# Performance work log

Measured on AMD Instinct MI355X. Metric: run time of the kernel, lower is better.

## Reference

```python
import jax, jax.numpy as jnp
import numpy as np

G = 56      # voxel grid side
N = 60000   # active voxels
K = 27      # 3x3x3 kernel offsets
CIN, COUT = 64, 96


def _build_kernel_map(seed=0):
    """Host-side hash-map neighbor search (what spnn does internally).
    Returns in_idx/out_idx of shape (K, N); padded entries have out_idx == N
    (scattered into a trash row) and in_idx == 0 (any valid gather index)."""
    rng = np.random.default_rng(seed)
    flat = rng.choice(G ** 3, size=N, replace=False)
    coords = np.stack(np.unravel_index(flat, (G, G, G)), axis=1)  # (N, 3)
    lut = -np.ones(G ** 3, dtype=np.int64)
    lut[flat] = np.arange(N)
    offs = np.array([(dx, dy, dz) for dx in (-1, 0, 1)
                     for dy in (-1, 0, 1) for dz in (-1, 0, 1)])
    in_idx = np.zeros((K, N), dtype=np.int32)
    out_idx = np.full((K, N), N, dtype=np.int32)
    for k in range(K):
        nb = coords + offs[k]
        ok = np.all((nb >= 0) & (nb < G), axis=1)
        fl = np.clip(nb[:, 0] * G * G + nb[:, 1] * G + nb[:, 2], 0, G ** 3 - 1)
        j = np.where(ok, lut[fl], -1)
        sel = np.nonzero(j >= 0)[0]
        m = sel.shape[0]
        out_idx[k, :m] = sel.astype(np.int32)       # output point i
        in_idx[k, :m] = j[sel].astype(np.int32)     # its neighbor at offset k
    return jnp.asarray(in_idx), jnp.asarray(out_idx)


def setup_inputs() -> dict:
    key = jax.random.key(0)
    ks = jax.random.split(key, 10)
    in_idx, out_idx = _build_kernel_map(0)
    s1 = 1.0 / np.sqrt(K * CIN)
    s2 = 1.0 / np.sqrt(K * COUT)
    return {
        "x":  jax.random.normal(ks[0], (N, CIN), jnp.float32),
        "W1": jax.random.normal(ks[1], (K, CIN, COUT), jnp.float32) * s1,
        "g1": jnp.ones((COUT,), jnp.float32),
        "b1": jnp.zeros((COUT,), jnp.float32),
        "m1": jax.random.normal(ks[2], (COUT,), jnp.float32) * 0.1,
        "v1": jax.random.uniform(ks[3], (COUT,), jnp.float32, 0.5, 1.5),
        "W2": jax.random.normal(ks[4], (K, COUT, COUT), jnp.float32) * s2,
        "g2": jnp.ones((COUT,), jnp.float32),
        "b2": jnp.zeros((COUT,), jnp.float32),
        "m2": jax.random.normal(ks[5], (COUT,), jnp.float32) * 0.1,
        "v2": jax.random.uniform(ks[6], (COUT,), jnp.float32, 0.5, 1.5),
        "Wd": jax.random.normal(ks[7], (CIN, COUT), jnp.float32) / np.sqrt(CIN),
        "gd": jnp.ones((COUT,), jnp.float32),
        "bd": jnp.zeros((COUT,), jnp.float32),
        "md": jax.random.normal(ks[8], (COUT,), jnp.float32) * 0.1,
        "vd": jax.random.uniform(ks[9], (COUT,), jnp.float32, 0.5, 1.5),
        "in_idx": in_idx,
        "out_idx": out_idx,
    }


def _bn(h, g, b, m, v, eps=1e-5):
    return (h - m) * (g * jax.lax.rsqrt(v + eps)) + b


def _sparse_conv(feat, W, in_idx, out_idx):
    # gather -> GEMM -> scatter-add, one pass per kernel offset.
    n = feat.shape[0]
    out = jnp.zeros((n + 1, W.shape[2]), feat.dtype)  # row n = trash row
    for k in range(W.shape[0]):
        out = out.at[out_idx[k]].add(feat[in_idx[k]] @ W[k])
    return out[:n]


def reference(x, W1, g1, b1, m1, v1, W2, g2, b2, m2, v2,
              Wd, gd, bd, md, vd, in_idx, out_idx):
    h = jax.nn.relu(_bn(_sparse_conv(x, W1, in_idx, out_idx), g1, b1, m1, v1))
    h = _bn(_sparse_conv(h, W2, in_idx, out_idx), g2, b2, m2, v2)
    skip = _bn(x @ Wd, gd, bd, md, vd)  # 1x1 conv downsample (inc != outc)
    return jax.nn.relu(h + skip)
```

## Files before the change

### kernel.cpp

```cpp
#include <hip/hip_runtime.h>


typedef __attribute__((ext_vector_type(8))) short bf16x8;
typedef __attribute__((ext_vector_type(4))) float f32x4;
typedef unsigned short u16;

constexpr int K27  = 27;
constexpr int CIN  = 64;
constexpr int COUT = 96;
constexpr int W1SZ = 6144;
constexpr int W2SZ = 9216;

#define MFMA __builtin_amdgcn_mfma_f32_16x16x32_bf16

__device__ __forceinline__ u16 f2bf(float f) {
  unsigned u = __float_as_uint(f);
  return (u16)((u + 0x7FFFu + ((u >> 16) & 1u)) >> 16);
}

__device__ __forceinline__ int posf(int c) {
  return ((c >> 2) & 3) * 8 + (c & 3) + ((c >> 4) & 1) * 4;
}

__device__ __forceinline__ bf16x8 ld16(const u16* p) {
  union { bf16x8 f; uint4 u; } r;
  r.u = *reinterpret_cast<const uint4*>(p);
  return r.f;
}

__device__ __forceinline__ void gll(const u16* g, u16* l) {
  __builtin_amdgcn_global_load_lds(
      (const __attribute__((address_space(1))) unsigned int*)g,
      (__attribute__((address_space(3))) unsigned int*)l, 16, 0, 0);
}

__device__ __forceinline__ void stage1(const u16* g, u16* l, int t) {
#pragma unroll
  for (int s = 0; s < 3; ++s) gll(g + s * 2048 + t * 8, l + s * 2048 + t * 8);
}

__device__ __forceinline__ void stage2(const u16* g, u16* l, int t) {
#pragma unroll
  for (int s = 0; s < 4; ++s) gll(g + s * 2048 + t * 8, l + s * 2048 + t * 8);
  if (t < 128) gll(g + 8192 + t * 8, l + 8192 + t * 8);
}

__device__ __forceinline__ int xcd_swz(int bid, int nblk) {
  int q = nblk >> 3, r = nblk & 7;
  int x = bid & 7, i = bid >> 3;
  return (x < r ? x * (q + 1) : r * (q + 1) + (x - r) * q) + i;
}

__global__ void build_nbT(const int* __restrict__ in_idx, const int* __restrict__ out_idx,
                          int* __restrict__ nbT, int N, int N_pad) {
  int t = blockIdx.x * blockDim.x + threadIdx.x;
  if (t >= K27 * N) return;
  int k = t / N;
  int o = out_idx[t];
  if (o < N) nbT[(size_t)k * N_pad + o] = in_idx[t];
}

__global__ void prep_all(
    const float* __restrict__ x, const float* __restrict__ W1,
    const float* __restrict__ W2, const float* __restrict__ Wd,
    const float* g1, const float* b1, const float* m1, const float* v1,
    const float* g2, const float* b2, const float* m2, const float* v2,
    const float* gd, const float* bd, const float* md, const float* vd,
    u16* __restrict__ xbf, u16* __restrict__ W1t, u16* __restrict__ W2t,
    u16* __restrict__ Wdt, float* __restrict__ bnc, u16* __restrict__ hbf, int N) {
  long i = (long)blockIdx.x * blockDim.x + threadIdx.x;
  const long R0 = (long)(N + 1) * CIN;
  const long R1 = (long)K27 * W1SZ;
  const long R2 = (long)K27 * W2SZ;
  const long R3 = (long)CIN * COUT;
  if (i < R0) {
    int c = (int)(i & 63);
    float v = (i < (long)N * CIN) ? x[i] : 0.f;
    xbf[(i & ~63L) + (c & 32) + posf(c & 31)] = f2bf(v);
    return;
  }
  i -= R0;
  if (i < R1) {
    int k = (int)(i / W1SZ), r = (int)(i % W1SZ);
    int f = r >> 9, lane = (r >> 3) & 63, j = r & 7;
    int c = f / 6, n = f % 6, m = lane & 15, g = lane >> 4;
    int co = n * 16 + m;
    int ci = c * 32 + 4 * g + (j & 3) + 16 * (j >> 2);
    W1t[i] = f2bf(W1[((size_t)k * CIN + ci) * COUT + co]);
    return;
  }
  i -= R1;
  if (i < R2) {
    int k = (int)(i / W2SZ), r = (int)(i % W2SZ);
    int f = r >> 9, lane = (r >> 3) & 63, j = r & 7;
    int c = f / 6, n = f % 6, m = lane & 15, g = lane >> 4;
    int co = n * 16 + m;
    int ci = c * 32 + 4 * g + (j & 3) + 16 * (j >> 2);
    W2t[i] = f2bf(W2[((size_t)k * COUT + ci) * COUT + co]);
    return;
  }
  i -= R2;
  if (i < R3) {
    int ci = (int)(i / COUT), co = (int)(i % COUT);
    Wdt[co * CIN + (ci & 32) + posf(ci & 31)] = f2bf(Wd[i]);
    return;
  }
  i -= R3;
  if (i < COUT) {
    int c = (int)i;
    float A1 = g1[c] * rsqrtf(v1[c] + 1e-5f);
    float A2 = g2[c] * rsqrtf(v2[c] + 1e-5f);
    float Ad = gd[c] * rsqrtf(vd[c] + 1e-5f);
    bnc[c]       = A1;
    bnc[96 + c]  = b1[c] - m1[c] * A1;
    bnc[192 + c] = A2;
    bnc[288 + c] = b2[c] - m2[c] * A2 + bd[c] - md[c] * Ad;
    bnc[384 + c] = Ad / A2;
    hbf[(size_t)N * COUT + c] = 0;
  }
}

__global__ __launch_bounds__(256, 2) void conv1_mfma(
    const u16* __restrict__ xbf, const u16* __restrict__ W1t,
    const int* __restrict__ nbT, const float* __restrict__ bnc,
    u16* __restrict__ hbf, int N, int N_pad) {
  __shared__ u16 Blds[2][W1SZ];
  const int t    = threadIdx.x;
  const int lane = t & 63;
  const int m    = lane & 15;
  const int slot = lane >> 4;
  const int so   = slot * 8;
  const int wid  = t >> 6;
  const int wr   = wid >> 1;
  const int wc   = wid & 1;
  const int bswz = xcd_swz(blockIdx.x, gridDim.x);
  const int roww = bswz * 64 + wr * 32;

  f32x4 acc[2][3];
#pragma unroll
  for (int s = 0; s < 2; ++s)
#pragma unroll
    for (int n = 0; n < 3; ++n) acc[s][n] = (f32x4){0.f, 0.f, 0.f, 0.f};

  const int* nbp = nbT + roww + m;

  stage1(W1t, Blds[0], t);
  int j1a = nbp[N_pad],               j1b = nbp[N_pad + 16];
  int j2a = nbp[2 * (size_t)N_pad],   j2b = nbp[2 * (size_t)N_pad + 16];
  bf16x8 Aa[2][2], Ab[2][2];
  {
    int j0a = nbp[0], j0b = nbp[16];
    const u16* pa = xbf + (size_t)(j0a < 0 ? N : j0a) * CIN + so;
    const u16* pb = xbf + (size_t)(j0b < 0 ? N : j0b) * CIN + so;
    Aa[0][0] = ld16(pa); Aa[0][1] = ld16(pa + 32);
    Aa[1][0] = ld16(pb); Aa[1][1] = ld16(pb + 32);
  }
  __syncthreads();

  auto step = [&](int k, bf16x8 (&Ac)[2][2], bf16x8 (&An)[2][2]) {
    const int cur = k & 1;
    if (k + 1 < K27) stage1(W1t + (size_t)(k + 1) * W1SZ, Blds[cur ^ 1], t);
    int j3a = 0, j3b = 0;
    if (k + 3 < K27) {
      j3a = nbp[(size_t)(k + 3) * N_pad];
      j3b = nbp[(size_t)(k + 3) * N_pad + 16];
    }
    if (k + 1 < K27) {
      const u16* pa = xbf + (size_t)(j1a < 0 ? N : j1a) * CIN + so;
      const u16* pb = xbf + (size_t)(j1b < 0 ? N : j1b) * CIN + so;
      An[0][0] = ld16(pa); An[0][1] = ld16(pa + 32);
      An[1][0] = ld16(pb); An[1][1] = ld16(pb + 32);
    }
    j1a = j2a; j1b = j2b; j2a = j3a; j2b = j3b;
    const u16* Bb = Blds[cur] + wc * 1536 + lane * 8;
#pragma unroll
    for (int c = 0; c < 2; ++c)
#pragma unroll
      for (int nn = 0; nn < 3; ++nn) {
        bf16x8 B = ld16(Bb + (c * 6 + nn) * 512);
        acc[0][nn] = MFMA(Ac[0][c], B, acc[0][nn], 0, 0, 0);
        acc[1][nn] = MFMA(Ac[1][c], B, acc[1][nn], 0, 0, 0);
      }
    __syncthreads();
  };

  for (int kk = 0; kk < K27 - 1; kk += 2) {
    step(kk, Aa, Ab);
    step(kk + 1, Ab, Aa);
  }
  step(K27 - 1, Aa, Ab);

  const int pbase = ((m >> 2) << 3) + (m & 3);
#pragma unroll
  for (int nn = 0; nn < 3; ++nn) {
    const int n   = wc * 3 + nn;
    const int col = n * 16 + m;
    const int dcol = (n >> 1) * 32 + pbase + ((n & 1) << 2);
    const float sc = bnc[col], bi = bnc[COUT + col];
#pragma unroll
    for (int s = 0; s < 2; ++s)
#pragma unroll
      for (int r = 0; r < 4; ++r) {
        const int row = roww + s * 16 + slot * 4 + r;
        if (row < N)
          hbf[(size_t)row * COUT + dcol] = f2bf(fmaxf(fmaf(acc[s][nn][r], sc, bi), 0.f));
      }
  }
}

__global__ __launch_bounds__(256, 2) void conv2_mfma(
    const u16* __restrict__ hbf, const u16* __restrict__ W2t,
    const u16* __restrict__ xbf, const u16* __restrict__ Wdt,
    const int* __restrict__ nbT, const float* __restrict__ bnc,
    float* __restrict__ out, int N, int N_pad) {
  __shared__ u16 Blds[2][W2SZ];
  const int t    = threadIdx.x;
  const int lane = t & 63;
  const int m    = lane & 15;
  const int slot = lane >> 4;
  const int so   = slot * 8;
  const int wid  = t >> 6;
  const int wr   = wid >> 1;
  const int wc   = wid & 1;
  const int bswz = xcd_swz(blockIdx.x, gridDim.x);
  const int roww = bswz * 64 + wr * 32;

  f32x4 acc[2][3];
#pragma unroll
  for (int s = 0; s < 2; ++s)
#pragma unroll
    for (int n = 0; n < 3; ++n) acc[s][n] = (f32x4){0.f, 0.f, 0.f, 0.f};

  stage2(W2t, Blds[0], t);

  {
    int r0 = roww + m, r1 = roww + 16 + m;
    const u16* pa = xbf + (size_t)(r0 < N ? r0 : N) * CIN + so;
    const u16* pb = xbf + (size_t)(r1 < N ? r1 : N) * CIN + so;
    bf16x8 S0a = ld16(pa), S1a = ld16(pa + 32);
    bf16x8 S0b = ld16(pb), S1b = ld16(pb + 32);
#pragma unroll
    for (int nn = 0; nn < 3; ++nn) {
      const int col = (wc * 3 + nn) * 16 + m;
      const u16* wd = Wdt + col * CIN + so;
      bf16x8 B0 = ld16(wd), B1 = ld16(wd + 32);
      acc[0][nn] = MFMA(S0a, B0, acc[0][nn], 0, 0, 0);
      acc[0][nn] = MFMA(S1a, B1, acc[0][nn], 0, 0, 0);
      acc[1][nn] = MFMA(S0b, B0, acc[1][nn], 0, 0, 0);
      acc[1][nn] = MFMA(S1b, B1, acc[1][nn], 0, 0, 0);
    }
#pragma unroll
    for (int nn = 0; nn < 3; ++nn) {
      float rr = bnc[384 + (wc * 3 + nn) * 16 + m];
      acc[0][nn] *= rr;
      acc[1][nn] *= rr;
    }
  }

  const int* nbp = nbT + roww + m;
  int j1a = nbp[N_pad],             j1b = nbp[N_pad + 16];
  int j2a = nbp[2 * (size_t)N_pad], j2b = nbp[2 * (size_t)N_pad + 16];
  bf16x8 Aa[2][3], Ab[2][3];
  {
    int j0a = nbp[0], j0b = nbp[16];
    const u16* pa = hbf + (size_t)(j0a < 0 ? N : j0a) * COUT + so;
    const u16* pb = hbf + (size_t)(j0b < 0 ? N : j0b) * COUT + so;
    Aa[0][0] = ld16(pa); Aa[0][1] = ld16(pa + 32); Aa[0][2] = ld16(pa + 64);
    Aa[1][0] = ld16(pb); Aa[1][1] = ld16(pb + 32); Aa[1][2] = ld16(pb + 64);
  }
  __syncthreads();

  auto step = [&](int k, bf16x8 (&Ac)[2][3], bf16x8 (&An)[2][3]) {
    const int cur = k & 1;
    if (k + 1 < K27) stage2(W2t + (size_t)(k + 1) * W2SZ, Blds[cur ^ 1], t);
    int j3a = 0, j3b = 0;
    if (k + 3 < K27) {
      j3a = nbp[(size_t)(k + 3) * N_pad];
      j3b = nbp[(size_t)(k + 3) * N_pad + 16];
    }
    if (k + 1 < K27) {
      const u16* pa = hbf + (size_t)(j1a < 0 ? N : j1a) * COUT + so;
      const u16* pb = hbf + (size_t)(j1b < 0 ? N : j1b) * COUT + so;
      An[0][0] = ld16(pa); An[0][1] = ld16(pa + 32); An[0][2] = ld16(pa + 64);
      An[1][0] = ld16(pb); An[1][1] = ld16(pb + 32); An[1][2] = ld16(pb + 64);
    }
    j1a = j2a; j1b = j2b; j2a = j3a; j2b = j3b;
    const u16* Bb = Blds[cur] + wc * 1536 + lane * 8;
#pragma unroll
    for (int c = 0; c < 3; ++c)
#pragma unroll
      for (int nn = 0; nn < 3; ++nn) {
        bf16x8 B = ld16(Bb + (c * 6 + nn) * 512);
        acc[0][nn] = MFMA(Ac[0][c], B, acc[0][nn], 0, 0, 0);
        acc[1][nn] = MFMA(Ac[1][c], B, acc[1][nn], 0, 0, 0);
      }
    __syncthreads();
  };

  for (int kk = 0; kk < K27 - 1; kk += 2) {
    step(kk, Aa, Ab);
    step(kk + 1, Ab, Aa);
  }
  step(K27 - 1, Aa, Ab);

#pragma unroll
  for (int nn = 0; nn < 3; ++nn) {
    const int col = (wc * 3 + nn) * 16 + m;
    const float sc = bnc[192 + col], bi = bnc[288 + col];
#pragma unroll
    for (int s = 0; s < 2; ++s)
#pragma unroll
      for (int r = 0; r < 4; ++r) {
        const int row = roww + s * 16 + slot * 4 + r;
        if (row < N)
          out[(size_t)row * COUT + col] = fmaxf(fmaf(acc[s][nn][r], sc, bi), 0.f);
      }
  }
}

extern "C" void kernel_launch(void* const* d_in, const int* in_sizes, int n_in,
                              void* d_out, int out_size, void* d_ws, size_t ws_size,
                              hipStream_t stream) {
  const float* x  = (const float*)d_in[0];
  const float* W1 = (const float*)d_in[1];
  const float* g1 = (const float*)d_in[2];
  const float* b1 = (const float*)d_in[3];
  const float* m1 = (const float*)d_in[4];
  const float* v1 = (const float*)d_in[5];
  const float* W2 = (const float*)d_in[6];
  const float* g2 = (const float*)d_in[7];
  const float* b2 = (const float*)d_in[8];
  const float* m2 = (const float*)d_in[9];
  const float* v2 = (const float*)d_in[10];
  const float* Wd = (const float*)d_in[11];
  const float* gd = (const float*)d_in[12];
  const float* bd = (const float*)d_in[13];
  const float* md = (const float*)d_in[14];
  const float* vd = (const float*)d_in[15];
  const int* in_idx  = (const int*)d_in[16];
  const int* out_idx = (const int*)d_in[17];

  const int N  = in_sizes[0] / CIN;
  const int GB = (N + 63) / 64;
  const int N_pad = GB * 64;

  char* ws = (char*)d_ws;
  size_t off = 0;
  auto alloc = [&](size_t bytes) { size_t o = off; off = (off + bytes + 255) & ~(size_t)255; return o; };
  int*   nbT = (int*)(ws + alloc((size_t)K27 * N_pad * sizeof(int)));
  u16*   xbf = (u16*)(ws + alloc((size_t)(N + 1) * CIN * sizeof(u16)));
  u16*   hbf = (u16*)(ws + alloc((size_t)(N + 1) * COUT * sizeof(u16)));
  u16*   W1t = (u16*)(ws + alloc((size_t)K27 * W1SZ * sizeof(u16)));
  u16*   W2t = (u16*)(ws + alloc((size_t)K27 * W2SZ * sizeof(u16)));
  u16*   Wdt = (u16*)(ws + alloc((size_t)COUT * CIN * sizeof(u16)));
  float* bnc = (float*)(ws + alloc(5 * 96 * sizeof(float)));

  hipMemsetAsync(nbT, 0xFF, (size_t)K27 * N_pad * sizeof(int), stream);
  build_nbT<<<(K27 * N + 255) / 256, 256, 0, stream>>>(in_idx, out_idx, nbT, N, N_pad);

  long ptotal = (long)(N + 1) * CIN + (long)K27 * W1SZ + (long)K27 * W2SZ +
                (long)CIN * COUT + COUT;
  prep_all<<<(int)((ptotal + 255) / 256), 256, 0, stream>>>(
      x, W1, W2, Wd, g1, b1, m1, v1, g2, b2, m2, v2, gd, bd, md, vd,
      xbf, W1t, W2t, Wdt, bnc, hbf, N);

  conv1_mfma<<<GB, 256, 0, stream>>>(xbf, W1t, nbT, bnc, hbf, N, N_pad);
  conv2_mfma<<<GB, 256, 0, stream>>>(hbf, W2t, xbf, Wdt, nbT, bnc, (float*)d_out, N, N_pad);
}
```

Before: 136.5 us.

## Replace full syncthreads with partial vmcnt waits and branchless padded prefetch pipeline

Replaces __syncthreads in the conv main loops with an explicit s_waitcnt vmcnt(N) plus s_barrier, so the next step's gather loads stay in flight across the barrier. Pads the neighbor table to 30 offsets and the weight buffers by one extra slice, which lets the k+1/k+3 guards be dropped and gives a branchless loop. Adds sched_barriers to pin instruction order. The hand-set vmcnt values depend on the exact load count per step (including stage1/stage2 global loads), so a wrong count could race on LDS. The padded weight slice is never initialised but is only staged and never used.

```diff
diff --git a/kernel.cpp b/kernel.cpp
--- a/kernel.cpp
+++ b/kernel.cpp
@@ -6,6 +6,7 @@
 typedef unsigned short u16;
 
 constexpr int K27  = 27;
+constexpr int KPAD = 30;
 constexpr int CIN  = 64;
 constexpr int COUT = 96;
 constexpr int W1SZ = 6144;
@@ -145,32 +146,34 @@
   const int* nbp = nbT + roww + m;
 
   stage1(W1t, Blds[0], t);
-  int j1a = nbp[N_pad],               j1b = nbp[N_pad + 16];
-  int j2a = nbp[2 * (size_t)N_pad],   j2b = nbp[2 * (size_t)N_pad + 16];
+  __builtin_amdgcn_sched_barrier(0);
+  int j1a, j1b, j2a, j2b;
   bf16x8 Aa[2][2], Ab[2][2];
   {
     int j0a = nbp[0], j0b = nbp[16];
+    j1a = nbp[N_pad];               j1b = nbp[N_pad + 16];
+    j2a = nbp[2 * (size_t)N_pad];   j2b = nbp[2 * (size_t)N_pad + 16];
     const u16* pa = xbf + (size_t)(j0a < 0 ? N : j0a) * CIN + so;
     const u16* pb = xbf + (size_t)(j0b < 0 ? N : j0b) * CIN + so;
     Aa[0][0] = ld16(pa); Aa[0][1] = ld16(pa + 32);
     Aa[1][0] = ld16(pb); Aa[1][1] = ld16(pb + 32);
   }
-  __syncthreads();
+  asm volatile("s_waitcnt vmcnt(6)" ::: "memory");
+  __builtin_amdgcn_s_barrier();
+  __builtin_amdgcn_sched_barrier(0);
 
   auto step = [&](int k, bf16x8 (&Ac)[2][2], bf16x8 (&An)[2][2]) {
     const int cur = k & 1;
-    if (k + 1 < K27) stage1(W1t + (size_t)(k + 1) * W1SZ, Blds[cur ^ 1], t);
-    int j3a = 0, j3b = 0;
-    if (k + 3 < K27) {
-      j3a = nbp[(size_t)(k + 3) * N_pad];
-      j3b = nbp[(size_t)(k + 3) * N_pad + 16];
-    }
-    if (k + 1 < K27) {
+    stage1(W1t + (size_t)(k + 1) * W1SZ, Blds[cur ^ 1], t);
+    __builtin_amdgcn_sched_barrier(0);
+    {
       const u16* pa = xbf + (size_t)(j1a < 0 ? N : j1a) * CIN + so;
       const u16* pb = xbf + (size_t)(j1b < 0 ? N : j1b) * CIN + so;
       An[0][0] = ld16(pa); An[0][1] = ld16(pa + 32);
       An[1][0] = ld16(pb); An[1][1] = ld16(pb + 32);
     }
+    int j3a = nbp[(size_t)(k + 3) * N_pad];
+    int j3b = nbp[(size_t)(k + 3) * N_pad + 16];
     j1a = j2a; j1b = j2b; j2a = j3a; j2b = j3b;
     const u16* Bb = Blds[cur] + wc * 1536 + lane * 8;
 #pragma unroll
@@ -181,7 +184,9 @@
         acc[0][nn] = MFMA(Ac[0][c], B, acc[0][nn], 0, 0, 0);
         acc[1][nn] = MFMA(Ac[1][c], B, acc[1][nn], 0, 0, 0);
       }
-    __syncthreads();
+    asm volatile("s_waitcnt vmcnt(6)" ::: "memory");
+    __builtin_amdgcn_s_barrier();
+    __builtin_amdgcn_sched_barrier(0);
   };
 
   for (int kk = 0; kk < K27 - 1; kk += 2) {
@@ -189,6 +194,8 @@
     step(kk + 1, Ab, Aa);
   }
   step(K27 - 1, Aa, Ab);
+  asm volatile("" :: "v"(Ab[0][0]), "v"(Ab[0][1]), "v"(Ab[1][0]), "v"(Ab[1][1]),
+                     "v"(j1a), "v"(j1b), "v"(j2a), "v"(j2b));
 
   const int pbase = ((m >> 2) << 3) + (m & 3);
 #pragma unroll
@@ -232,7 +239,7 @@
     for (int n = 0; n < 3; ++n) acc[s][n] = (f32x4){0.f, 0.f, 0.f, 0.f};
 
   stage2(W2t, Blds[0], t);
-
+  __builtin_amdgcn_sched_barrier(0);
   {
     int r0 = roww + m, r1 = roww + 16 + m;
     const u16* pa = xbf + (size_t)(r0 < N ? r0 : N) * CIN + so;
@@ -258,32 +265,33 @@
   }
 
   const int* nbp = nbT + roww + m;
-  int j1a = nbp[N_pad],             j1b = nbp[N_pad + 16];
-  int j2a = nbp[2 * (size_t)N_pad], j2b = nbp[2 * (size_t)N_pad + 16];
+  int j1a, j1b, j2a, j2b;
   bf16x8 Aa[2][3], Ab[2][3];
   {
     int j0a = nbp[0], j0b = nbp[16];
+    j1a = nbp[N_pad];               j1b = nbp[N_pad + 16];
+    j2a = nbp[2 * (size_t)N_pad];   j2b = nbp[2 * (size_t)N_pad + 16];
     const u16* pa = hbf + (size_t)(j0a < 0 ? N : j0a) * COUT + so;
     const u16* pb = hbf + (size_t)(j0b < 0 ? N : j0b) * COUT + so;
     Aa[0][0] = ld16(pa); Aa[0][1] = ld16(pa + 32); Aa[0][2] = ld16(pa + 64);
     Aa[1][0] = ld16(pb); Aa[1][1] = ld16(pb + 32); Aa[1][2] = ld16(pb + 64);
   }
-  __syncthreads();
+  asm volatile("s_waitcnt vmcnt(8)" ::: "memory");
+  __builtin_amdgcn_s_barrier();
+  __builtin_amdgcn_sched_barrier(0);
 
   auto step = [&](int k, bf16x8 (&Ac)[2][3], bf16x8 (&An)[2][3]) {
     const int cur = k & 1;
-    if (k + 1 < K27) stage2(W2t + (size_t)(k + 1) * W2SZ, Blds[cur ^ 1], t);
-    int j3a = 0, j3b = 0;
-    if (k + 3 < K27) {
-      j3a = nbp[(size_t)(k + 3) * N_pad];
-      j3b = nbp[(size_t)(k + 3) * N_pad + 16];
-    }
-    if (k + 1 < K27) {
+    stage2(W2t + (size_t)(k + 1) * W2SZ, Blds[cur ^ 1], t);
+    __builtin_amdgcn_sched_barrier(0);
+    {
       const u16* pa = hbf + (size_t)(j1a < 0 ? N : j1a) * COUT + so;
       const u16* pb = hbf + (size_t)(j1b < 0 ? N : j1b) * COUT + so;
       An[0][0] = ld16(pa); An[0][1] = ld16(pa + 32); An[0][2] = ld16(pa + 64);
       An[1][0] = ld16(pb); An[1][1] = ld16(pb + 32); An[1][2] = ld16(pb + 64);
     }
+    int j3a = nbp[(size_t)(k + 3) * N_pad];
+    int j3b = nbp[(size_t)(k + 3) * N_pad + 16];
     j1a = j2a; j1b = j2b; j2a = j3a; j2b = j3b;
     const u16* Bb = Blds[cur] + wc * 1536 + lane * 8;
 #pragma unroll
@@ -294,7 +302,9 @@
         acc[0][nn] = MFMA(Ac[0][c], B, acc[0][nn], 0, 0, 0);
         acc[1][nn] = MFMA(Ac[1][c], B, acc[1][nn], 0, 0, 0);
       }
-    __syncthreads();
+    asm volatile("s_waitcnt vmcnt(8)" ::: "memory");
+    __builtin_amdgcn_s_barrier();
+    __builtin_amdgcn_sched_barrier(0);
   };
 
   for (int kk = 0; kk < K27 - 1; kk += 2) {
@@ -302,6 +312,9 @@
     step(kk + 1, Ab, Aa);
   }
   step(K27 - 1, Aa, Ab);
+  asm volatile("" :: "v"(Ab[0][0]), "v"(Ab[0][1]), "v"(Ab[0][2]),
+                     "v"(Ab[1][0]), "v"(Ab[1][1]), "v"(Ab[1][2]),
+                     "v"(j1a), "v"(j1b), "v"(j2a), "v"(j2b));
 
 #pragma unroll
   for (int nn = 0; nn < 3; ++nn) {
@@ -347,15 +360,15 @@
   char* ws = (char*)d_ws;
   size_t off = 0;
   auto alloc = [&](size_t bytes) { size_t o = off; off = (off + bytes + 255) & ~(size_t)255; return o; };
-  int*   nbT = (int*)(ws + alloc((size_t)K27 * N_pad * sizeof(int)));
+  int*   nbT = (int*)(ws + alloc((size_t)KPAD * N_pad * sizeof(int)));
   u16*   xbf = (u16*)(ws + alloc((size_t)(N + 1) * CIN * sizeof(u16)));
   u16*   hbf = (u16*)(ws + alloc((size_t)(N + 1) * COUT * sizeof(u16)));
-  u16*   W1t = (u16*)(ws + alloc((size_t)K27 * W1SZ * sizeof(u16)));
-  u16*   W2t = (u16*)(ws + alloc((size_t)K27 * W2SZ * sizeof(u16)));
+  u16*   W1t = (u16*)(ws + alloc((size_t)(K27 + 1) * W1SZ * sizeof(u16)));
+  u16*   W2t = (u16*)(ws + alloc((size_t)(K27 + 1) * W2SZ * sizeof(u16)));
   u16*   Wdt = (u16*)(ws + alloc((size_t)COUT * CIN * sizeof(u16)));
   float* bnc = (float*)(ws + alloc(5 * 96 * sizeof(float)));
 
-  hipMemsetAsync(nbT, 0xFF, (size_t)K27 * N_pad * sizeof(int), stream);
+  hipMemsetAsync(nbT, 0xFF, (size_t)KPAD * N_pad * sizeof(int), stream);
   build_nbT<<<(K27 * N + 255) / 256, 256, 0, stream>>>(in_idx, out_idx, nbT, N, N_pad);
 
   long ptotal = (long)(N + 1) * CIN + (long)K27 * W1SZ + (long)K27 * W2SZ +
```

Measured after the change: 138.8 us. Within noise of the previous version (+1.8%).

## Stage gathered A rows into swizzled LDS via async global_load_lds

Applied to the files above, without the earlier changes.

Replaces the per-lane register prefetch of gathered neighbor rows with asynchronous global-to-LDS loads into an XOR-swizzled shared tile, then reads the A fragments from LDS for the MFMAs. The neighbor table is padded to 32 offsets so index prefetch two steps ahead needs no bounds check, and the hbf zero row is extended for the padded column chunks. It also raises wave priority around the MFMA block. The aim is to cut register pressure and issue the irregular gathers as wide coalesced async copies, at the cost of an extra barrier per offset step and more LDS use.

```diff
diff --git a/kernel.cpp b/kernel.cpp
--- a/kernel.cpp
+++ b/kernel.cpp
@@ -6,6 +6,7 @@
 typedef unsigned short u16;
 
 constexpr int K27  = 27;
+constexpr int KPAD = 32;
 constexpr int CIN  = 64;
 constexpr int COUT = 96;
 constexpr int W1SZ = 6144;
@@ -32,17 +33,6 @@
   __builtin_amdgcn_global_load_lds(
       (const __attribute__((address_space(1))) unsigned int*)g,
       (__attribute__((address_space(3))) unsigned int*)l, 16, 0, 0);
-}
-
-__device__ __forceinline__ void stage1(const u16* g, u16* l, int t) {
-#pragma unroll
-  for (int s = 0; s < 3; ++s) gll(g + s * 2048 + t * 8, l + s * 2048 + t * 8);
-}
-
-__device__ __forceinline__ void stage2(const u16* g, u16* l, int t) {
-#pragma unroll
-  for (int s = 0; s < 4; ++s) gll(g + s * 2048 + t * 8, l + s * 2048 + t * 8);
-  if (t < 128) gll(g + 8192 + t * 8, l + 8192 + t * 8);
 }
 
 __device__ __forceinline__ int xcd_swz(int bid, int nblk) {
@@ -106,17 +96,19 @@
     return;
   }
   i -= R3;
-  if (i < COUT) {
-    int c = (int)i;
-    float A1 = g1[c] * rsqrtf(v1[c] + 1e-5f);
-    float A2 = g2[c] * rsqrtf(v2[c] + 1e-5f);
-    float Ad = gd[c] * rsqrtf(vd[c] + 1e-5f);
-    bnc[c]       = A1;
-    bnc[96 + c]  = b1[c] - m1[c] * A1;
-    bnc[192 + c] = A2;
-    bnc[288 + c] = b2[c] - m2[c] * A2 + bd[c] - md[c] * Ad;
-    bnc[384 + c] = Ad / A2;
-    hbf[(size_t)N * COUT + c] = 0;
+  if (i < 128) {
+    hbf[(size_t)N * COUT + i] = 0;
+    if (i < COUT) {
+      int c = (int)i;
+      float A1 = g1[c] * rsqrtf(v1[c] + 1e-5f);
+      float A2 = g2[c] * rsqrtf(v2[c] + 1e-5f);
+      float Ad = gd[c] * rsqrtf(vd[c] + 1e-5f);
+      bnc[c]       = A1;
+      bnc[96 + c]  = b1[c] - m1[c] * A1;
+      bnc[192 + c] = A2;
+      bnc[288 + c] = b2[c] - m2[c] * A2 + bd[c] - md[c] * Ad;
+      bnc[384 + c] = Ad / A2;
+    }
   }
 }
 
@@ -124,17 +116,17 @@
     const u16* __restrict__ xbf, const u16* __restrict__ W1t,
     const int* __restrict__ nbT, const float* __restrict__ bnc,
     u16* __restrict__ hbf, int N, int N_pad) {
-  __shared__ u16 Blds[2][W1SZ];
+  __shared__ u16 Ab[4096];
+  __shared__ u16 Bb[2][W1SZ];
   const int t    = threadIdx.x;
   const int lane = t & 63;
   const int m    = lane & 15;
   const int slot = lane >> 4;
-  const int so   = slot * 8;
-  const int wid  = t >> 6;
-  const int wr   = wid >> 1;
-  const int wc   = wid & 1;
-  const int bswz = xcd_swz(blockIdx.x, gridDim.x);
-  const int roww = bswz * 64 + wr * 32;
+  const int w    = t >> 6;
+  const int wr   = w >> 1;
+  const int wc   = w & 1;
+  const int row0 = xcd_swz(blockIdx.x, gridDim.x) * 64;
+  const int roww = row0 + wr * 32;
 
   f32x4 acc[2][3];
 #pragma unroll
@@ -142,53 +134,76 @@
 #pragma unroll
     for (int n = 0; n < 3; ++n) acc[s][n] = (f32x4){0.f, 0.f, 0.f, 0.f};
 
-  const int* nbp = nbT + roww + m;
-
-  stage1(W1t, Blds[0], t);
-  int j1a = nbp[N_pad],               j1b = nbp[N_pad + 16];
-  int j2a = nbp[2 * (size_t)N_pad],   j2b = nbp[2 * (size_t)N_pad + 16];
-  bf16x8 Aa[2][2], Ab[2][2];
-  {
-    int j0a = nbp[0], j0b = nbp[16];
-    const u16* pa = xbf + (size_t)(j0a < 0 ? N : j0a) * CIN + so;
-    const u16* pb = xbf + (size_t)(j0b < 0 ? N : j0b) * CIN + so;
-    Aa[0][0] = ld16(pa); Aa[0][1] = ld16(pa + 32);
-    Aa[1][0] = ld16(pb); Aa[1][1] = ld16(pb + 32);
-  }
+  int rA[2], qsw[2];
+#pragma unroll
+  for (int i = 0; i < 2; ++i) {
+    int c = (w * 2 + i) * 64 + lane;
+    int r = c >> 3;
+    rA[i]  = r;
+    qsw[i] = ((c & 7) ^ (r & 7)) * 8;
+  }
+
+  auto loadJ = [&](int kt, int (&jd)[2]) {
+#pragma unroll
+    for (int i = 0; i < 2; ++i) jd[i] = nbT[(size_t)kt * N_pad + row0 + rA[i]];
+  };
+  auto stageA = [&](int (&jc)[2]) {
+#pragma unroll
+    for (int i = 0; i < 2; ++i) {
+      int j = jc[i];
+      const u16* src = xbf + (size_t)(j < 0 ? N : j) * CIN + qsw[i];
+      gll(src, (u16*)Ab + (w * 2 + i) * 512);
+    }
+  };
+  auto stageB = [&](int kt) {
+#pragma unroll
+    for (int s = 0; s < 3; ++s)
+      gll(W1t + (size_t)kt * W1SZ + s * 2048 + t * 8, &Bb[kt & 1][s * 2048 + t * 8]);
+  };
+  auto compute = [&](int k) {
+    const u16* Bc = Bb[k & 1] + wc * 1536 + lane * 8;
+    bf16x8 av[2][2];
+#pragma unroll
+    for (int s = 0; s < 2; ++s) {
+      const int row = wr * 32 + s * 16 + m;
+      const u16* ar = (const u16*)Ab + row * 64;
+      const int rx = row & 7;
+#pragma unroll
+      for (int c = 0; c < 2; ++c) av[s][c] = ld16(ar + ((slot + c * 4) ^ rx) * 8);
+    }
+    __builtin_amdgcn_s_setprio(1);
+#pragma unroll
+    for (int c = 0; c < 2; ++c)
+#pragma unroll
+      for (int nn = 0; nn < 3; ++nn) {
+        bf16x8 B = ld16(Bc + (c * 6 + nn) * 512);
+        acc[0][nn] = MFMA(av[0][c], B, acc[0][nn], 0, 0, 0);
+        acc[1][nn] = MFMA(av[1][c], B, acc[1][nn], 0, 0, 0);
+      }
+    __builtin_amdgcn_s_setprio(0);
+  };
+
+  int jA[2], jB[2];
+  loadJ(0, jA);
+  stageB(0);
+  stageA(jA);
+  loadJ(1, jA);
   __syncthreads();
 
-  auto step = [&](int k, bf16x8 (&Ac)[2][2], bf16x8 (&An)[2][2]) {
-    const int cur = k & 1;
-    if (k + 1 < K27) stage1(W1t + (size_t)(k + 1) * W1SZ, Blds[cur ^ 1], t);
-    int j3a = 0, j3b = 0;
-    if (k + 3 < K27) {
-      j3a = nbp[(size_t)(k + 3) * N_pad];
-      j3b = nbp[(size_t)(k + 3) * N_pad + 16];
-    }
-    if (k + 1 < K27) {
-      const u16* pa = xbf + (size_t)(j1a < 0 ? N : j1a) * CIN + so;
-      const u16* pb = xbf + (size_t)(j1b < 0 ? N : j1b) * CIN + so;
-      An[0][0] = ld16(pa); An[0][1] = ld16(pa + 32);
-      An[1][0] = ld16(pb); An[1][1] = ld16(pb + 32);
-    }
-    j1a = j2a; j1b = j2b; j2a = j3a; j2b = j3b;
-    const u16* Bb = Blds[cur] + wc * 1536 + lane * 8;
-#pragma unroll
-    for (int c = 0; c < 2; ++c)
-#pragma unroll
-      for (int nn = 0; nn < 3; ++nn) {
-        bf16x8 B = ld16(Bb + (c * 6 + nn) * 512);
-        acc[0][nn] = MFMA(Ac[0][c], B, acc[0][nn], 0, 0, 0);
-        acc[1][nn] = MFMA(Ac[1][c], B, acc[1][nn], 0, 0, 0);
-      }
+  auto step = [&](int k, int (&jc)[2], int (&jn)[2]) {
+    if (k + 1 < K27) stageB(k + 1);
+    loadJ(k + 2, jn);
+    compute(k);
     __syncthreads();
+    if (k + 1 < K27) stageA(jc);
+    __syncthreads();
   };
 
   for (int kk = 0; kk < K27 - 1; kk += 2) {
-    step(kk, Aa, Ab);
-    step(kk + 1, Ab, Aa);
-  }
-  step(K27 - 1, Aa, Ab);
+    step(kk,     jA, jB);
+    step(kk + 1, jB, jA);
+  }
+  step(K27 - 1, jA, jB);
 
   const int pbase = ((m >> 2) << 3) + (m & 3);
 #pragma unroll
@@ -213,17 +228,17 @@
     const u16* __restrict__ xbf, const u16* __restrict__ Wdt,
     const int* __restrict__ nbT, const float* __restrict__ bnc,
     float* __restrict__ out, int N, int N_pad) {
-  __shared__ u16 Blds[2][W2SZ];
+  __shared__ u16 Ab[8192];
+  __shared__ u16 Bb[2][W2SZ];
   const int t    = threadIdx.x;
   const int lane = t & 63;
   const int m    = lane & 15;
   const int slot = lane >> 4;
-  const int so   = slot * 8;
-  const int wid  = t >> 6;
-  const int wr   = wid >> 1;
-  const int wc   = wid & 1;
-  const int bswz = xcd_swz(blockIdx.x, gridDim.x);
-  const int roww = bswz * 64 + wr * 32;
+  const int w    = t >> 6;
+  const int wr   = w >> 1;
+  const int wc   = w & 1;
+  const int row0 = xcd_swz(blockIdx.x, gridDim.x) * 64;
+  const int roww = row0 + wr * 32;
 
   f32x4 acc[2][3];
 #pragma unroll
@@ -231,18 +246,76 @@
 #pragma unroll
     for (int n = 0; n < 3; ++n) acc[s][n] = (f32x4){0.f, 0.f, 0.f, 0.f};
 
-  stage2(W2t, Blds[0], t);
+  int rA[4], qsw[4], inv[4];
+#pragma unroll
+  for (int i = 0; i < 4; ++i) {
+    int c = (w * 4 + i) * 64 + lane;
+    int r = c >> 4;
+    int q = (c & 15) ^ (r & 7);
+    rA[i]  = r;
+    qsw[i] = q * 8;
+    inv[i] = (q >= 12);
+  }
+
+  auto loadJ = [&](int kt, int (&jd)[4]) {
+#pragma unroll
+    for (int i = 0; i < 4; ++i) jd[i] = nbT[(size_t)kt * N_pad + row0 + rA[i]];
+  };
+  auto stageA = [&](int (&jc)[4]) {
+#pragma unroll
+    for (int i = 0; i < 4; ++i) {
+      int j = jc[i];
+      int sel = (j < 0 || inv[i]) ? N : j;
+      const u16* src = hbf + (size_t)sel * COUT + qsw[i];
+      gll(src, (u16*)Ab + (w * 4 + i) * 512);
+    }
+  };
+  auto stageB = [&](int kt) {
+    const u16* src = W2t + (size_t)kt * W2SZ;
+    u16* dst = Bb[kt & 1];
+#pragma unroll
+    for (int s = 0; s < 4; ++s) gll(src + s * 2048 + t * 8, dst + s * 2048 + t * 8);
+    if (t < 128) gll(src + 8192 + t * 8, dst + 8192 + t * 8);
+  };
+  auto compute = [&](int k) {
+    const u16* Bc = Bb[k & 1] + wc * 1536 + lane * 8;
+    bf16x8 av[2][3];
+#pragma unroll
+    for (int s = 0; s < 2; ++s) {
+      const int row = wr * 32 + s * 16 + m;
+      const u16* ar = (const u16*)Ab + row * 128;
+      const int rx = row & 7;
+#pragma unroll
+      for (int c = 0; c < 3; ++c) av[s][c] = ld16(ar + ((slot + c * 4) ^ rx) * 8);
+    }
+    __builtin_amdgcn_s_setprio(1);
+#pragma unroll
+    for (int c = 0; c < 3; ++c)
+#pragma unroll
+      for (int nn = 0; nn < 3; ++nn) {
+        bf16x8 B = ld16(Bc + (c * 6 + nn) * 512);
+        acc[0][nn] = MFMA(av[0][c], B, acc[0][nn], 0, 0, 0);
+        acc[1][nn] = MFMA(av[1][c], B, acc[1][nn], 0, 0, 0);
+      }
+    __builtin_amdgcn_s_setprio(0);
+  };
+
+  int jA[4], jB[4];
+  loadJ(0, jA);
+  stageB(0);
+  stageA(jA);
+  loadJ(1, jA);
 
   {
     int r0 = roww + m, r1 = roww + 16 + m;
-    const u16* pa = xbf + (size_t)(r0 < N ? r0 : N) * CIN + so;
-    const u16* pb = xbf + (size_t)(r1 < N ? r1 : N) * CIN + so;
+    const u16* pa = xbf + (size_t)(r0 < N ? r0 : N) * CIN + slot * 8;
+    const u16* pb = xbf + (size_t)(r1 < N ? r1 : N) * CIN + slot * 8;
     bf16x8 S0a = ld16(pa), S1a = ld16(pa + 32);
     bf16x8 S0b = ld16(pb), S1b = ld16(pb + 32);
 #pragma unroll
     for (int nn = 0; nn < 3; ++nn) {
       const int col = (wc * 3 + nn) * 16 + m;
-      const u16* wd = Wdt + col * CIN + so;
+      const u16* wd = Wdt + col * CIN + slot * 8;
       bf16x8 B0 = ld16(wd), B1 = ld16(wd + 32);
       acc[0][nn] = MFMA(S0a, B0, acc[0][nn], 0, 0, 0);
       acc[0][nn] = MFMA(S1a, B1, acc[0][nn], 0, 0, 0);
@@ -256,52 +329,22 @@
       acc[1][nn] *= rr;
     }
   }
-
-  const int* nbp = nbT + roww + m;
-  int j1a = nbp[N_pad],             j1b = nbp[N_pad + 16];
-  int j2a = nbp[2 * (size_t)N_pad], j2b = nbp[2 * (size_t)N_pad + 16];
-  bf16x8 Aa[2][3], Ab[2][3];
-  {
-    int j0a = nbp[0], j0b = nbp[16];
-    const u16* pa = hbf + (size_t)(j0a < 0 ? N : j0a) * COUT + so;
-    const u16* pb = hbf + (size_t)(j0b < 0 ? N : j0b) * COUT + so;
-    Aa[0][0] = ld16(pa); Aa[0][1] = ld16(pa + 32); Aa[0][2] = ld16(pa + 64);
-    Aa[1][0] = ld16(pb); Aa[1][1] = ld16(pb + 32); Aa[1][2] = ld16(pb + 64);
-  }
   __syncthreads();
 
-  auto step = [&](int k, bf16x8 (&Ac)[2][3], bf16x8 (&An)[2][3]) {
-    const int cur = k & 1;
-    if (k + 1 < K27) stage2(W2t + (size_t)(k + 1) * W2SZ, Blds[cur ^ 1], t);
-    int j3a = 0, j3b = 0;
-    if (k + 3 < K27) {
-      j3a = nbp[(size_t)(k + 3) * N_pad];
-      j3b = nbp[(size_t)(k + 3) * N_pad + 16];
-    }
-    if (k + 1 < K27) {
-      const u16* pa = hbf + (size_t)(j1a < 0 ? N : j1a) * COUT + so;
-      const u16* pb = hbf + (size_t)(j1b < 0 ? N : j1b) * COUT + so;
-      An[0][0] = ld16(pa); An[0][1] = ld16(pa + 32); An[0][2] = ld16(pa + 64);
-      An[1][0] = ld16(pb); An[1][1] = ld16(pb + 32); An[1][2] = ld16(pb + 64);
-    }
-    j1a = j2a; j1b = j2b; j2a = j3a; j2b = j3b;
-    const u16* Bb = Blds[cur] + wc * 1536 + lane * 8;
-#pragma unroll
-    for (int c = 0; c < 3; ++c)
-#pragma unroll
-      for (int nn = 0; nn < 3; ++nn) {
-        bf16x8 B = ld16(Bb + (c * 6 + nn) * 512);
-        acc[0][nn] = MFMA(Ac[0][c], B, acc[0][nn], 0, 0, 0);
-        acc[1][nn] = MFMA(Ac[1][c], B, acc[1][nn], 0, 0, 0);
-      }
+  auto step = [&](int k, int (&jc)[4], int (&jn)[4]) {
+    if (k + 1 < K27) stageB(k + 1);
+    loadJ(k + 2, jn);
+    compute(k);
     __syncthreads();
+    if (k + 1 < K27) stageA(jc);
+    __syncthreads();
   };
 
   for (int kk = 0; kk < K27 - 1; kk += 2) {
-    step(kk, Aa, Ab);
-    step(kk + 1, Ab, Aa);
-  }
-  step(K27 - 1, Aa, Ab);
+    step(kk,     jA, jB);
+    step(kk + 1, jB, jA);
+  }
+  step(K27 - 1, jA, jB);
 
 #pragma unroll
   for (int nn = 0; nn < 3; ++nn) {
@@ -347,19 +390,19 @@
   char* ws = (char*)d_ws;
   size_t off = 0;
   auto alloc = [&](size_t bytes) { size_t o = off; off = (off + bytes + 255) & ~(size_t)255; return o; };
-  int*   nbT = (int*)(ws + alloc((size_t)K27 * N_pad * sizeof(int)));
+  int*   nbT = (int*)(ws + alloc((size_t)KPAD * N_pad * sizeof(int)));
   u16*   xbf = (u16*)(ws + alloc((size_t)(N + 1) * CIN * sizeof(u16)));
-  u16*   hbf = (u16*)(ws + alloc((size_t)(N + 1) * COUT * sizeof(u16)));
+  u16*   hbf = (u16*)(ws + alloc((size_t)(N + 2) * COUT * sizeof(u16)));
   u16*   W1t = (u16*)(ws + alloc((size_t)K27 * W1SZ * sizeof(u16)));
   u16*   W2t = (u16*)(ws + alloc((size_t)K27 * W2SZ * sizeof(u16)));
   u16*   Wdt = (u16*)(ws + alloc((size_t)COUT * CIN * sizeof(u16)));
   float* bnc = (float*)(ws + alloc(5 * 96 * sizeof(float)));
 
-  hipMemsetAsync(nbT, 0xFF, (size_t)K27 * N_pad * sizeof(int), stream);
+  hipMemsetAsync(nbT, 0xFF, (size_t)KPAD * N_pad * sizeof(int), stream);
   build_nbT<<<(K27 * N + 255) / 256, 256, 0, stream>>>(in_idx, out_idx, nbT, N, N_pad);
 
   long ptotal = (long)(N + 1) * CIN + (long)K27 * W1SZ + (long)K27 * W2SZ +
-                (long)CIN * COUT + COUT;
+                (long)CIN * COUT + 128;
   prep_all<<<(int)((ptotal + 255) / 256), 256, 0, stream>>>(
       x, W1, W2, Wd, g1, b1, m1, v1, g2, b2, m2, v2, gd, bd, md, vd,
       xbf, W1t, W2t, Wdt, bnc, hbf, N);
```

After: 132.7 us. -2.8%, faster.
